# Kernel optimization log

Hardware: AMD Instinct MI355X
Metric: run time of the kernel (lower is better)

## Reference

```python
import math
import jax, jax.numpy as jnp
import numpy as np

B, S, D, H = 4, 2048, 768, 12
HD = D // H  # 64


def setup_inputs() -> dict:
    key = jax.random.key(0)
    ks = jax.random.split(key, 10)
    sc = 0.02
    return {
        "hidden_states": jax.random.normal(ks[0], (B, S, D), dtype=jnp.float32),
        "attention_mask": jax.random.randint(ks[1], (1, H, S, S), 0, 2).astype(jnp.bool_),
        "q_w": jax.random.normal(ks[2], (D, D), dtype=jnp.float32) * sc,
        "q_b": jax.random.normal(ks[3], (D,), dtype=jnp.float32) * sc,
        "k_w": jax.random.normal(ks[4], (D, D), dtype=jnp.float32) * sc,
        "k_b": jax.random.normal(ks[5], (D,), dtype=jnp.float32) * sc,
        "v_w": jax.random.normal(ks[6], (D, D), dtype=jnp.float32) * sc,
        "v_b": jax.random.normal(ks[7], (D,), dtype=jnp.float32) * sc,
        "out_w": jax.random.normal(ks[8], (D, D), dtype=jnp.float32) * sc,
        "out_b": jax.random.normal(ks[9], (D,), dtype=jnp.float32) * sc,
    }


def _split_heads(x):
    # [B, S, D] -> [B, H, S, HD]
    b, s, _ = x.shape
    return x.reshape(b, s, H, HD).transpose(0, 2, 1, 3)


def reference(hidden_states, attention_mask, q_w, q_b, k_w, k_b, v_w, v_b, out_w, out_b):
    q = _split_heads(hidden_states @ q_w.T + q_b)
    k = _split_heads(hidden_states @ k_w.T + k_b)
    v = _split_heads(hidden_states @ v_w.T + v_b)
    scores = jnp.einsum("bhqd,bhkd->bhqk", q, k) / math.sqrt(HD)
    # prune_mode, before softmax: masked_fill(~mask, -inf)
    scores = jnp.where(attention_mask, scores, -jnp.inf)
    probs = jax.nn.softmax(scores, axis=-1)  # [B, H, S, S]
    ctx = jnp.einsum("bhqk,bhkd->bhqd", probs, v)
    ctx = ctx.transpose(0, 2, 1, 3).reshape(hidden_states.shape[0], -1, D)
    return ctx @ out_w.T + out_b
```

## Files before the change

### kernel.cpp

```cpp
#include <hip/hip_runtime.h>
#include <hip/hip_bf16.h>

#define B_ 4
#define S_ 2048
#define D_ 768
#define H_ 12
#define HD_ 64

typedef __attribute__((ext_vector_type(8))) short bf16x8;
typedef __attribute__((ext_vector_type(4))) float floatx4;

#define QSCALE 0.18033688011112042f

__device__ __forceinline__ unsigned short f2bf(float x) {
    union { float f; unsigned int u; } v; v.f = x;
    unsigned int r = v.u + 0x7fffu + ((v.u >> 16) & 1u);
    return (unsigned short)(r >> 16);
}

__device__ __forceinline__ unsigned int pk2bf(float a, float b) {
    __hip_bfloat162 h = __float22bfloat162_rn(make_float2(a, b));
    unsigned int u;
    __builtin_memcpy(&u, &h, 4);
    return u;
}

__device__ __forceinline__ void gload_lds16(const void* g, void* l) {
    __builtin_amdgcn_global_load_lds(
        (const __attribute__((address_space(1))) unsigned int*)g,
        (__attribute__((address_space(3))) unsigned int*)l, 16, 0, 0);
}

__device__ __forceinline__ bf16x8 ld_b64x2(const unsigned short* p) {
    union { bf16x8 v; unsigned long long q[2]; } u;
    u.q[0] = *(const unsigned long long*)p;
    u.q[1] = *(const unsigned long long*)(p + 4);
    return u.v;
}

__global__ void prep(const float* __restrict__ hs,
                     const float* __restrict__ w0, const float* __restrict__ w1,
                     const float* __restrict__ w2, const float* __restrict__ w3,
                     const int* __restrict__ mask,
                     unsigned short* __restrict__ Xb,
                     unsigned short* __restrict__ Wb,
                     unsigned long long* __restrict__ bits) {
    int bid = blockIdx.x;
    int t = threadIdx.x;
    if (bid < 6144) {
        int i = bid * 256 + t;
        float4 f = ((const float4*)hs)[i];
        ushort4 o;
        o.x = f2bf(f.x); o.y = f2bf(f.y); o.z = f2bf(f.z); o.w = f2bf(f.w);
        ((ushort4*)Xb)[i] = o;
    } else if (bid < 8448) {
        int q = bid - 6144;
        int wid = q / 576;
        const float* src = (wid == 0) ? w0 : (wid == 1) ? w1 : (wid == 2) ? w2 : w3;
        unsigned short* d = Wb + (size_t)wid * 589824;
        int i = (q - wid * 576) * 256 + t;
        float4 f = ((const float4*)src)[i];
        ushort4 o;
        o.x = f2bf(f.x); o.y = f2bf(f.y); o.z = f2bf(f.z); o.w = f2bf(f.w);
        ((ushort4*)d)[i] = o;
    } else {
        size_t gw = ((size_t)(bid - 8448) * 256 + t) >> 6;
        int lane = t & 63;
        size_t base = gw * 256;
        unsigned long long b0 = __ballot(mask[base + lane] != 0);
        unsigned long long b1 = __ballot(mask[base + 64 + lane] != 0);
        unsigned long long b2 = __ballot(mask[base + 128 + lane] != 0);
        unsigned long long b3 = __ballot(mask[base + 192 + lane] != 0);
        if (lane == 0) {
            bits[gw * 4 + 0] = b0; bits[gw * 4 + 1] = b1;
            bits[gw * 4 + 2] = b2; bits[gw * 4 + 3] = b3;
        }
    }
}

__global__ __launch_bounds__(256) void qkv_gemm(
    const unsigned short* __restrict__ Xb,
    const unsigned short* __restrict__ Wq, const unsigned short* __restrict__ Wk,
    const unsigned short* __restrict__ Wv,
    const float* __restrict__ bq, const float* __restrict__ bk,
    const float* __restrict__ bv,
    unsigned short* __restrict__ Qo, unsigned short* __restrict__ Ko,
    unsigned short* __restrict__ Vo)
{
    const int z = blockIdx.z;
    const unsigned short* W = (z == 0) ? Wq : (z == 1) ? Wk : Wv;
    const float* bias = (z == 0) ? bq : (z == 1) ? bk : bv;
    unsigned short* Out = (z == 0) ? Qo : (z == 1) ? Ko : Vo;
    const float scale = (z == 0) ? QSCALE : 1.0f;

    const int m0 = blockIdx.x * 128;
    const int n0 = blockIdx.y * 128;

    __shared__ alignas(16) unsigned short SMall[16384];
    unsigned short* SM = SMall;

    const int t = threadIdx.x;
    const int lane = t & 63, w = t >> 6;
    const int c = lane & 15, quad = lane >> 4;
    const int wm = (w & 1) * 64, wn = (w >> 1) * 64;

    const int srowq = lane >> 2, sc8 = (lane & 3) * 8;

    floatx4 acc[4][4];
#pragma unroll
    for (int i = 0; i < 4; i++)
#pragma unroll
        for (int j = 0; j < 4; j++) acc[i][j] = (floatx4){0.f, 0.f, 0.f, 0.f};

#pragma unroll
    for (int i = 0; i < 2; i++) {
        int chunk = i * 4 + w;
        int row = chunk * 16 + srowq;
        gload_lds16(&Xb[(size_t)(m0 + row) * 768 + sc8], &SMall[chunk * 512]);
        gload_lds16(&W [(size_t)(n0 + row) * 768 + sc8], &SMall[4096 + chunk * 512]);
    }

    for (int it = 0; it < 24; it++) {
        const int cur = it & 1;
        __syncthreads();
        if (it + 1 < 24) {
            int k1 = (it + 1) * 32;
#pragma unroll
            for (int i = 0; i < 2; i++) {
                int chunk = i * 4 + w;
                int row = chunk * 16 + srowq;
                gload_lds16(&Xb[(size_t)(m0 + row) * 768 + k1 + sc8],
                            &SMall[(cur ^ 1) * 8192 + chunk * 512]);
                gload_lds16(&W [(size_t)(n0 + row) * 768 + k1 + sc8],
                            &SMall[(cur ^ 1) * 8192 + 4096 + chunk * 512]);
            }
        }
        const unsigned short* As = &SMall[cur * 8192];
        const unsigned short* Bs = As + 4096;
        bf16x8 a[4], b[4];
#pragma unroll
        for (int i = 0; i < 4; i++)
            a[i] = *(const bf16x8*)&As[(wm + i * 16 + c) * 32 + quad * 8];
#pragma unroll
        for (int j = 0; j < 4; j++)
            b[j] = *(const bf16x8*)&Bs[(wn + j * 16 + c) * 32 + quad * 8];
#pragma unroll
        for (int i = 0; i < 4; i++)
#pragma unroll
            for (int j = 0; j < 4; j++)
                acc[i][j] = __builtin_amdgcn_mfma_f32_16x16x32_bf16(
                    a[i], b[j], acc[i][j], 0, 0, 0);
    }
    __syncthreads();

    const int bb = m0 >> 11, ssb = m0 & 2047;
    if (z == 2) {
#pragma unroll
        for (int half = 0; half < 2; half++) {
            if ((w >> 1) == half) {
#pragma unroll
                for (int j = 0; j < 4; j++) {
                    int n_l = j * 16 + c;
                    float bias_n = bias[n0 + half * 64 + n_l];
#pragma unroll
                    for (int i = 0; i < 4; i++) {
#pragma unroll
                        for (int r = 0; r < 4; r++) {
                            int m = wm + i * 16 + quad * 4 + r;
                            int ms = m ^ (c << 3);
                            SM[n_l * 128 + ms] = f2bf(acc[i][j][r] + bias_n);
                        }
                    }
                }
            }
            __syncthreads();
#pragma unroll
            for (int rb = 0; rb < 2; rb++) {
                int n_l = (t >> 3) + rb * 32;
                int ch = t & 7;
                int n_abs = n0 + half * 64 + n_l;
                int hh = n_abs >> 6, dd = n_abs & 63;
                unsigned short* dst =
                    Out + (((size_t)(bb * H_ + hh)) * 64 + dd) * S_ + ssb;
#pragma unroll
                for (int p = 0; p < 2; p++) {
                    int mc = ch + p * 8;
                    uint4 v = *(const uint4*)&SM[n_l * 128 + ((mc ^ (n_l & 15)) * 8)];
                    *(uint4*)&dst[mc * 8] = v;
                }
            }
            __syncthreads();
        }
    } else {
#pragma unroll
        for (int half = 0; half < 2; half++) {
            if ((w >> 1) == half) {
#pragma unroll
                for (int j = 0; j < 4; j++) {
                    float bias_n = bias[n0 + half * 64 + j * 16 + c];
#pragma unroll
                    for (int i = 0; i < 4; i++) {
#pragma unroll
                        for (int r = 0; r < 4; r++) {
                            int m = wm + i * 16 + quad * 4 + r;
                            int chunk = (j * 2 + (c >> 3)) ^ ((m >> 1) & 7);
                            SM[m * 64 + chunk * 8 + (c & 7)] =
                                f2bf((acc[i][j][r] + bias_n) * scale);
                        }
                    }
                }
            }
            __syncthreads();
            {
                int hh = (n0 >> 6) + half;
                unsigned short* dst =
                    Out + ((size_t)(bb * H_ + hh) * S_ + ssb) * 64;
#pragma unroll
                for (int i = 0; i < 4; i++) {
                    int idx = i * 256 + t;
                    int m = idx >> 3, ch = idx & 7;
                    uint4 v = *(const uint4*)&SM[m * 64 + ((ch ^ ((m >> 1) & 7)) * 8)];
                    *(uint4*)&dst[(size_t)m * 64 + ch * 8] = v;
                }
            }
            __syncthreads();
        }
    }
}

__global__ __launch_bounds__(256) void out_gemm(
    const unsigned short* __restrict__ Cb, const unsigned short* __restrict__ Wo,
    const float* __restrict__ bo, float* __restrict__ out)
{
    const int m0 = blockIdx.x * 64;
    const int n0 = blockIdx.y * 128;

    __shared__ alignas(16) unsigned short SMall[12288];

    const int t = threadIdx.x;
    const int lane = t & 63, w = t >> 6;
    const int c = lane & 15, quad = lane >> 4;
    const int wm = (w & 1) * 32, wn = (w >> 1) * 64;

    const int arow = w * 16 + (lane >> 2);
    const int brow0 = (lane >> 2);
    const int sc8 = (lane & 3) * 8;

    floatx4 acc[2][4];
#pragma unroll
    for (int i = 0; i < 2; i++)
#pragma unroll
        for (int j = 0; j < 4; j++) acc[i][j] = (floatx4){0.f, 0.f, 0.f, 0.f};

    gload_lds16(&Cb[(size_t)(m0 + arow) * 768 + sc8], &SMall[w * 512]);
#pragma unroll
    for (int i = 0; i < 2; i++) {
        int chunk = i * 4 + w;
        gload_lds16(&Wo[(size_t)(n0 + chunk * 16 + brow0) * 768 + sc8],
                    &SMall[2048 + chunk * 512]);
    }

    for (int it = 0; it < 24; it++) {
        const int cur = it & 1;
        __syncthreads();
        if (it + 1 < 24) {
            int k1 = (it + 1) * 32;
            gload_lds16(&Cb[(size_t)(m0 + arow) * 768 + k1 + sc8],
                        &SMall[(cur ^ 1) * 6144 + w * 512]);
#pragma unroll
            for (int i = 0; i < 2; i++) {
                int chunk = i * 4 + w;
                gload_lds16(&Wo[(size_t)(n0 + chunk * 16 + brow0) * 768 + k1 + sc8],
                            &SMall[(cur ^ 1) * 6144 + 2048 + chunk * 512]);
            }
        }
        const unsigned short* As = &SMall[cur * 6144];
        const unsigned short* Bs = As + 2048;
        bf16x8 a[2], b[4];
#pragma unroll
        for (int i = 0; i < 2; i++)
            a[i] = *(const bf16x8*)&As[(wm + i * 16 + c) * 32 + quad * 8];
#pragma unroll
        for (int j = 0; j < 4; j++)
            b[j] = *(const bf16x8*)&Bs[(wn + j * 16 + c) * 32 + quad * 8];
#pragma unroll
        for (int i = 0; i < 2; i++)
#pragma unroll
            for (int j = 0; j < 4; j++)
                acc[i][j] = __builtin_amdgcn_mfma_f32_16x16x32_bf16(
                    a[i], b[j], acc[i][j], 0, 0, 0);
    }
    __syncthreads();

    float* SMf = (float*)SMall;
#pragma unroll
    for (int qtr = 0; qtr < 4; qtr++) {
        if ((w >> 1) == (qtr >> 1)) {
#pragma unroll
            for (int jj = 0; jj < 2; jj++) {
                int j = (qtr & 1) * 2 + jj;
                float bias_n = bo[n0 + wn + j * 16 + c];
                int chunk = jj * 4 + (c >> 2);
#pragma unroll
                for (int i = 0; i < 2; i++) {
#pragma unroll
                    for (int r = 0; r < 4; r++) {
                        int m = wm + i * 16 + quad * 4 + r;
                        SMf[m * 32 + ((chunk ^ (m & 7)) * 4) + (c & 3)] =
                            acc[i][j][r] + bias_n;
                    }
                }
            }
        }
        __syncthreads();
#pragma unroll
        for (int i = 0; i < 2; i++) {
            int idx = i * 256 + t;
            int m = idx >> 3, ch = idx & 7;
            float4 v = *(const float4*)&SMf[m * 32 + ((ch ^ (m & 7)) * 4)];
            *(float4*)&out[(size_t)(m0 + m) * 768 + n0 + qtr * 32 + ch * 4] = v;
        }
        __syncthreads();
    }
}

__global__ __launch_bounds__(256) void attn(
    const unsigned short* __restrict__ Q, const unsigned short* __restrict__ K,
    const unsigned short* __restrict__ Vt,
    const unsigned long long* __restrict__ mbits,
    unsigned short* __restrict__ ctx)
{
    const int qt = blockIdx.x;
    const int bh = blockIdx.y;
    const int b = bh / H_, h = bh % H_;

    const unsigned short* Qp = Q + (size_t)bh * S_ * 64 + (size_t)qt * 128 * 64;
    const unsigned short* Kp = K + (size_t)bh * S_ * 64;
    const unsigned short* Vp = Vt + (size_t)bh * 64 * S_;

    __shared__ alignas(16) unsigned short Ks[2][64 * 64];
    __shared__ alignas(16) unsigned short Vs[2][64 * 64];
    __shared__ alignas(16) unsigned short Ps[4][16 * 68];

    const int t = threadIdx.x;
    const int lane = t & 63, w = t >> 6;
    const int c = lane & 15, quad = lane >> 4;

    bf16x8 aq[2][2];
#pragma unroll
    for (int st = 0; st < 2; st++) {
        aq[st][0] = *(const bf16x8*)&Qp[(size_t)(w * 32 + st * 16 + c) * 64 + quad * 8];
        aq[st][1] = *(const bf16x8*)&Qp[(size_t)(w * 32 + st * 16 + c) * 64 + 32 + quad * 8];
    }

    const unsigned long long* mrow =
        mbits + ((size_t)h * S_ + qt * 128 + w * 32 + quad * 4) * (S_ / 64);

    floatx4 acc_o[2][4];
#pragma unroll
    for (int st = 0; st < 2; st++)
#pragma unroll
        for (int i = 0; i < 4; i++) acc_o[st][i] = (floatx4){0.f, 0.f, 0.f, 0.f};
    float lp[2][4] = {{0.f, 0.f, 0.f, 0.f}, {0.f, 0.f, 0.f, 0.f}};

    const int srow = (lane >> 3);
    const int rc0 = ((quad     ) ^ (c & 7)) * 8;
    const int rc1 = ((quad + 4) ^ (c & 7)) * 8;

#pragma unroll
    for (int i = 0; i < 2; i++) {
        int chunk = i * 4 + w;
        int row = chunk * 8 + srow;
        int col8 = (((lane & 7) ^ ((row >> 2) & 7))) * 8;
        gload_lds16(&Kp[(size_t)row * 64 + col8], &Ks[0][chunk * 512]);
        gload_lds16(&Vp[(size_t)row * S_ + col8], &Vs[0][chunk * 512]);
    }

    for (int kt = 0; kt < S_ / 64; kt++) {
        const int cur = kt & 1;
        __syncthreads();
        if (kt + 1 < S_ / 64) {
#pragma unroll
            for (int i = 0; i < 2; i++) {
                int chunk = i * 4 + w;
                int row = chunk * 8 + srow;
                int col8 = (((lane & 7) ^ ((row >> 2) & 7))) * 8;
                gload_lds16(&Kp[(size_t)((kt + 1) * 64 + row) * 64 + col8],
                            &Ks[cur ^ 1][chunk * 512]);
                gload_lds16(&Vp[(size_t)row * S_ + (kt + 1) * 64 + col8],
                            &Vs[cur ^ 1][chunk * 512]);
            }
        }

#pragma unroll
        for (int st = 0; st < 2; st++) {
            floatx4 sacc[4];
#pragma unroll
            for (int nt = 0; nt < 4; nt++) {
                int kr = 4 * c + nt;
                bf16x8 bk0 = *(const bf16x8*)&Ks[cur][kr * 64 + rc0];
                bf16x8 bk1 = *(const bf16x8*)&Ks[cur][kr * 64 + rc1];
                floatx4 zz = (floatx4){0.f, 0.f, 0.f, 0.f};
                zz = __builtin_amdgcn_mfma_f32_16x16x32_bf16(aq[st][0], bk0, zz, 0, 0, 0);
                zz = __builtin_amdgcn_mfma_f32_16x16x32_bf16(aq[st][1], bk1, zz, 0, 0, 0);
                sacc[nt] = zz;
            }

            asm volatile("" ::: "memory");
#pragma unroll
            for (int r = 0; r < 4; r++) {
                unsigned int nib =
                    (unsigned int)(mrow[st * 16 * (S_ / 64) + r * (S_ / 64) + kt] >> (4 * c)) & 15u;
                float p0 = (nib & 1u) ? __builtin_amdgcn_exp2f(sacc[0][r]) : 0.f;
                float p1 = (nib & 2u) ? __builtin_amdgcn_exp2f(sacc[1][r]) : 0.f;
                float p2 = (nib & 4u) ? __builtin_amdgcn_exp2f(sacc[2][r]) : 0.f;
                float p3 = (nib & 8u) ? __builtin_amdgcn_exp2f(sacc[3][r]) : 0.f;
                lp[st][r] += (p0 + p1) + (p2 + p3);
                unsigned long long pk =
                    (unsigned long long)pk2bf(p0, p1) |
                    ((unsigned long long)pk2bf(p2, p3) << 32);
                *(unsigned long long*)&Ps[w][(quad * 4 + r) * 68 + 4 * c] = pk;
            }
            asm volatile("" ::: "memory");

            bf16x8 ap0 = ld_b64x2(&Ps[w][c * 68 + quad * 8]);
            bf16x8 ap1 = ld_b64x2(&Ps[w][c * 68 + 32 + quad * 8]);
#pragma unroll
            for (int nt = 0; nt < 4; nt++) {
                int vr = 4 * c + nt;
                bf16x8 bv0 = *(const bf16x8*)&Vs[cur][vr * 64 + rc0];
                bf16x8 bv1 = *(const bf16x8*)&Vs[cur][vr * 64 + rc1];
                acc_o[st][nt] = __builtin_amdgcn_mfma_f32_16x16x32_bf16(ap0, bv0, acc_o[st][nt], 0, 0, 0);
                acc_o[st][nt] = __builtin_amdgcn_mfma_f32_16x16x32_bf16(ap1, bv1, acc_o[st][nt], 0, 0, 0);
            }
        }
    }

#pragma unroll
    for (int st = 0; st < 2; st++)
#pragma unroll
        for (int r = 0; r < 4; r++) {
            float s = lp[st][r];
#pragma unroll
            for (int o = 1; o < 16; o <<= 1) s += __shfl_xor(s, o, 64);
            lp[st][r] = s;
        }

#pragma unroll
    for (int st = 0; st < 2; st++)
#pragma unroll
        for (int nt = 0; nt < 4; nt++)
#pragma unroll
            for (int r = 0; r < 4; r++) {
                int qrow = qt * 128 + w * 32 + st * 16 + quad * 4 + r;
                int dd = 4 * c + nt;
                float v = acc_o[st][nt][r] / lp[st][r];
                ctx[((size_t)b * S_ + qrow) * 768 + h * 64 + dd] = f2bf(v);
            }
}

extern "C" void kernel_launch(void* const* d_in, const int* in_sizes, int n_in,
                              void* d_out, int out_size, void* d_ws, size_t ws_size,
                              hipStream_t stream) {
    const float* hs    = (const float*)d_in[0];
    const int*   mask  = (const int*)d_in[1];
    const float* q_w   = (const float*)d_in[2];
    const float* q_b   = (const float*)d_in[3];
    const float* k_w   = (const float*)d_in[4];
    const float* k_b   = (const float*)d_in[5];
    const float* v_w   = (const float*)d_in[6];
    const float* v_b   = (const float*)d_in[7];
    const float* out_w = (const float*)d_in[8];
    const float* out_b = (const float*)d_in[9];
    float* out = (float*)d_out;

    unsigned short* Xb  = (unsigned short*)d_ws;
    unsigned short* Wqb = Xb + 6291456;
    unsigned short* Wkb = Wqb + 589824;
    unsigned short* Wvb = Wkb + 589824;
    unsigned short* Wob = Wvb + 589824;
    unsigned short* Qb  = Wob + 589824;
    unsigned short* Kb  = Qb + 6291456;
    unsigned short* Vtb = Kb + 6291456;
    unsigned short* Cb  = Vtb + 6291456;
    unsigned long long* mbits = (unsigned long long*)(Cb + 6291456);

    prep<<<57600, 256, 0, stream>>>(hs, q_w, k_w, v_w, out_w, mask, Xb, Wqb, mbits);
    qkv_gemm<<<dim3(64, 6, 3), 256, 0, stream>>>(Xb, Wqb, Wkb, Wvb,
                                                 q_b, k_b, v_b, Qb, Kb, Vtb);
    attn<<<dim3(16, 48), 256, 0, stream>>>(Qb, Kb, Vtb, mbits, Cb);
    out_gemm<<<dim3(128, 6), 256, 0, stream>>>(Cb, Wob, out_b, out);
}
```

Baseline: 483.7 us.

## Share K/V LDS fragments across both subtiles and raise priority around MFMA

Swaps the loop order so each K and V fragment read from LDS feeds both 16-row subtiles, halving LDS reads for K/V. The P buffer gets a slot per subtile, so both softmax tiles are written before the PV MFMAs run. s_setprio brackets the MFMA clusters to favour matrix issue across waves. The cost is more live registers (sacc[2][4], ap[2][2]), which may lower occupancy, plus extra LDS for the doubled P buffer.

```diff
diff --git a/kernel.cpp b/kernel.cpp
--- a/kernel.cpp
+++ b/kernel.cpp
@@ -340,7 +340,7 @@
 
     __shared__ alignas(16) unsigned short Ks[2][64 * 64];
     __shared__ alignas(16) unsigned short Vs[2][64 * 64];
-    __shared__ alignas(16) unsigned short Ps[4][16 * 68];
+    __shared__ alignas(16) unsigned short Ps[4][2][16 * 68];
 
     const int t = threadIdx.x;
     const int lane = t & 63, w = t >> 6;
@@ -392,48 +392,63 @@
             }
         }
 
-#pragma unroll
-        for (int st = 0; st < 2; st++) {
-            floatx4 sacc[4];
-#pragma unroll
-            for (int nt = 0; nt < 4; nt++) {
-                int kr = 4 * c + nt;
-                bf16x8 bk0 = *(const bf16x8*)&Ks[cur][kr * 64 + rc0];
-                bf16x8 bk1 = *(const bf16x8*)&Ks[cur][kr * 64 + rc1];
+        floatx4 sacc[2][4];
+        __builtin_amdgcn_s_setprio(1);
+#pragma unroll
+        for (int nt = 0; nt < 4; nt++) {
+            int kr = 4 * c + nt;
+            bf16x8 bk0 = *(const bf16x8*)&Ks[cur][kr * 64 + rc0];
+            bf16x8 bk1 = *(const bf16x8*)&Ks[cur][kr * 64 + rc1];
+#pragma unroll
+            for (int st = 0; st < 2; st++) {
                 floatx4 zz = (floatx4){0.f, 0.f, 0.f, 0.f};
                 zz = __builtin_amdgcn_mfma_f32_16x16x32_bf16(aq[st][0], bk0, zz, 0, 0, 0);
                 zz = __builtin_amdgcn_mfma_f32_16x16x32_bf16(aq[st][1], bk1, zz, 0, 0, 0);
-                sacc[nt] = zz;
-            }
-
-            asm volatile("" ::: "memory");
+                sacc[st][nt] = zz;
+            }
+        }
+        __builtin_amdgcn_s_setprio(0);
+
+        asm volatile("" ::: "memory");
+#pragma unroll
+        for (int st = 0; st < 2; st++) {
 #pragma unroll
             for (int r = 0; r < 4; r++) {
                 unsigned int nib =
                     (unsigned int)(mrow[st * 16 * (S_ / 64) + r * (S_ / 64) + kt] >> (4 * c)) & 15u;
-                float p0 = (nib & 1u) ? __builtin_amdgcn_exp2f(sacc[0][r]) : 0.f;
-                float p1 = (nib & 2u) ? __builtin_amdgcn_exp2f(sacc[1][r]) : 0.f;
-                float p2 = (nib & 4u) ? __builtin_amdgcn_exp2f(sacc[2][r]) : 0.f;
-                float p3 = (nib & 8u) ? __builtin_amdgcn_exp2f(sacc[3][r]) : 0.f;
+                float p0 = (nib & 1u) ? __builtin_amdgcn_exp2f(sacc[st][0][r]) : 0.f;
+                float p1 = (nib & 2u) ? __builtin_amdgcn_exp2f(sacc[st][1][r]) : 0.f;
+                float p2 = (nib & 4u) ? __builtin_amdgcn_exp2f(sacc[st][2][r]) : 0.f;
+                float p3 = (nib & 8u) ? __builtin_amdgcn_exp2f(sacc[st][3][r]) : 0.f;
                 lp[st][r] += (p0 + p1) + (p2 + p3);
                 unsigned long long pk =
                     (unsigned long long)pk2bf(p0, p1) |
                     ((unsigned long long)pk2bf(p2, p3) << 32);
-                *(unsigned long long*)&Ps[w][(quad * 4 + r) * 68 + 4 * c] = pk;
-            }
-            asm volatile("" ::: "memory");
-
-            bf16x8 ap0 = ld_b64x2(&Ps[w][c * 68 + quad * 8]);
-            bf16x8 ap1 = ld_b64x2(&Ps[w][c * 68 + 32 + quad * 8]);
-#pragma unroll
-            for (int nt = 0; nt < 4; nt++) {
-                int vr = 4 * c + nt;
-                bf16x8 bv0 = *(const bf16x8*)&Vs[cur][vr * 64 + rc0];
-                bf16x8 bv1 = *(const bf16x8*)&Vs[cur][vr * 64 + rc1];
-                acc_o[st][nt] = __builtin_amdgcn_mfma_f32_16x16x32_bf16(ap0, bv0, acc_o[st][nt], 0, 0, 0);
-                acc_o[st][nt] = __builtin_amdgcn_mfma_f32_16x16x32_bf16(ap1, bv1, acc_o[st][nt], 0, 0, 0);
-            }
-        }
+                *(unsigned long long*)&Ps[w][st][(quad * 4 + r) * 68 + 4 * c] = pk;
+            }
+        }
+        asm volatile("" ::: "memory");
+
+        bf16x8 ap[2][2];
+#pragma unroll
+        for (int st = 0; st < 2; st++) {
+            ap[st][0] = ld_b64x2(&Ps[w][st][c * 68 + quad * 8]);
+            ap[st][1] = ld_b64x2(&Ps[w][st][c * 68 + 32 + quad * 8]);
+        }
+
+        __builtin_amdgcn_s_setprio(1);
+#pragma unroll
+        for (int nt = 0; nt < 4; nt++) {
+            int vr = 4 * c + nt;
+            bf16x8 bv0 = *(const bf16x8*)&Vs[cur][vr * 64 + rc0];
+            bf16x8 bv1 = *(const bf16x8*)&Vs[cur][vr * 64 + rc1];
+#pragma unroll
+            for (int st = 0; st < 2; st++) {
+                acc_o[st][nt] = __builtin_amdgcn_mfma_f32_16x16x32_bf16(ap[st][0], bv0, acc_o[st][nt], 0, 0, 0);
+                acc_o[st][nt] = __builtin_amdgcn_mfma_f32_16x16x32_bf16(ap[st][1], bv1, acc_o[st][nt], 0, 0, 0);
+            }
+        }
+        __builtin_amdgcn_s_setprio(0);
     }
 
 #pragma unroll
```

After: 497.0 us. 1.03x slower.

## Prefetch mask bits, swizzle P buffer, and raise priority around MFMA blocks

Applied to the files above, without the earlier changes.

Mask words for the next key tile are loaded into registers one iteration ahead, so the global-load latency overlaps with the current tile's compute instead of stalling the softmax step. The P staging buffer drops its 68-element padded stride for an XOR-swizzled 64-element layout, which allows single 128-bit LDS reads in place of two 64-bit reads. s_setprio is raised around the MFMA sections to favour matrix issue across waves. The cost is extra registers for the mask prefetch, which could lower occupancy.

```diff
diff --git a/kernel.cpp b/kernel.cpp
--- a/kernel.cpp
+++ b/kernel.cpp
@@ -29,13 +29,6 @@
     __builtin_amdgcn_global_load_lds(
         (const __attribute__((address_space(1))) unsigned int*)g,
         (__attribute__((address_space(3))) unsigned int*)l, 16, 0, 0);
-}
-
-__device__ __forceinline__ bf16x8 ld_b64x2(const unsigned short* p) {
-    union { bf16x8 v; unsigned long long q[2]; } u;
-    u.q[0] = *(const unsigned long long*)p;
-    u.q[1] = *(const unsigned long long*)(p + 4);
-    return u.v;
 }
 
 __global__ void prep(const float* __restrict__ hs,
@@ -340,7 +333,7 @@
 
     __shared__ alignas(16) unsigned short Ks[2][64 * 64];
     __shared__ alignas(16) unsigned short Vs[2][64 * 64];
-    __shared__ alignas(16) unsigned short Ps[4][16 * 68];
+    __shared__ alignas(16) unsigned short Ps[4][16 * 64];
 
     const int t = threadIdx.x;
     const int lane = t & 63, w = t >> 6;
@@ -366,6 +359,13 @@
     const int srow = (lane >> 3);
     const int rc0 = ((quad     ) ^ (c & 7)) * 8;
     const int rc1 = ((quad + 4) ^ (c & 7)) * 8;
+
+    unsigned long long mcur[2][4];
+#pragma unroll
+    for (int st = 0; st < 2; st++)
+#pragma unroll
+        for (int r = 0; r < 4; r++)
+            mcur[st][r] = mrow[st * 512 + r * 32];
 
 #pragma unroll
     for (int i = 0; i < 2; i++) {
@@ -379,6 +379,7 @@
     for (int kt = 0; kt < S_ / 64; kt++) {
         const int cur = kt & 1;
         __syncthreads();
+        unsigned long long mnext[2][4];
         if (kt + 1 < S_ / 64) {
 #pragma unroll
             for (int i = 0; i < 2; i++) {
@@ -390,11 +391,22 @@
                 gload_lds16(&Vp[(size_t)row * S_ + (kt + 1) * 64 + col8],
                             &Vs[cur ^ 1][chunk * 512]);
             }
+#pragma unroll
+            for (int st = 0; st < 2; st++)
+#pragma unroll
+                for (int r = 0; r < 4; r++)
+                    mnext[st][r] = mrow[st * 512 + r * 32 + kt + 1];
+        } else {
+#pragma unroll
+            for (int st = 0; st < 2; st++)
+#pragma unroll
+                for (int r = 0; r < 4; r++) mnext[st][r] = 0ull;
         }
 
 #pragma unroll
         for (int st = 0; st < 2; st++) {
             floatx4 sacc[4];
+            __builtin_amdgcn_s_setprio(1);
 #pragma unroll
             for (int nt = 0; nt < 4; nt++) {
                 int kr = 4 * c + nt;
@@ -405,12 +417,12 @@
                 zz = __builtin_amdgcn_mfma_f32_16x16x32_bf16(aq[st][1], bk1, zz, 0, 0, 0);
                 sacc[nt] = zz;
             }
+            __builtin_amdgcn_s_setprio(0);
 
             asm volatile("" ::: "memory");
 #pragma unroll
             for (int r = 0; r < 4; r++) {
-                unsigned int nib =
-                    (unsigned int)(mrow[st * 16 * (S_ / 64) + r * (S_ / 64) + kt] >> (4 * c)) & 15u;
+                unsigned int nib = (unsigned int)(mcur[st][r] >> (4 * c)) & 15u;
                 float p0 = (nib & 1u) ? __builtin_amdgcn_exp2f(sacc[0][r]) : 0.f;
                 float p1 = (nib & 2u) ? __builtin_amdgcn_exp2f(sacc[1][r]) : 0.f;
                 float p2 = (nib & 4u) ? __builtin_amdgcn_exp2f(sacc[2][r]) : 0.f;
@@ -419,12 +431,16 @@
                 unsigned long long pk =
                     (unsigned long long)pk2bf(p0, p1) |
                     ((unsigned long long)pk2bf(p2, p3) << 32);
-                *(unsigned long long*)&Ps[w][(quad * 4 + r) * 68 + 4 * c] = pk;
+                int row = quad * 4 + r;
+                *(unsigned long long*)&Ps[w][row * 64 +
+                    (((c >> 1) ^ (row & 7)) << 3) + ((c & 1) << 2)] = pk;
             }
             asm volatile("" ::: "memory");
 
-            bf16x8 ap0 = ld_b64x2(&Ps[w][c * 68 + quad * 8]);
-            bf16x8 ap1 = ld_b64x2(&Ps[w][c * 68 + 32 + quad * 8]);
+            bf16x8 ap0 = *(const bf16x8*)&Ps[w][c * 64 + ((quad ^ (c & 7)) << 3)];
+            bf16x8 ap1 = *(const bf16x8*)&Ps[w][c * 64 + (((quad + 4) ^ (c & 7)) << 3)];
+
+            __builtin_amdgcn_s_setprio(1);
 #pragma unroll
             for (int nt = 0; nt < 4; nt++) {
                 int vr = 4 * c + nt;
@@ -433,7 +449,13 @@
                 acc_o[st][nt] = __builtin_amdgcn_mfma_f32_16x16x32_bf16(ap0, bv0, acc_o[st][nt], 0, 0, 0);
                 acc_o[st][nt] = __builtin_amdgcn_mfma_f32_16x16x32_bf16(ap1, bv1, acc_o[st][nt], 0, 0, 0);
             }
-        }
+            __builtin_amdgcn_s_setprio(0);
+        }
+
+#pragma unroll
+        for (int st = 0; st < 2; st++)
+#pragma unroll
+            for (int r = 0; r < 4; r++) mcur[st][r] = mnext[st][r];
     }
 
 #pragma unroll
```

Result: slower. 515.4 us (+6.6%).
